# Optimization experiments

Hardware: AMD Instinct MI355X
Metric: run time of the kernel (lower is better)

The kernel has to match this reference:

```python
import jax, jax.numpy as jnp
import numpy as np

NT, NE = 2, 2            # node types, edge types
N, FIN, HID = 50000, 128, 128
H, D, L, E = 4, 32, 2, 400000
EDGE_SRC = (0, 1)        # edge type e: src node type
EDGE_DST = (1, 0)        # edge type e: dst node type


def _segment_softmax(scores, seg, n):
    # scores: [E, H], softmax over edges sharing the same dst node
    m = jax.ops.segment_max(scores, seg, num_segments=n)
    e = jnp.exp(scores - m[seg])
    s = jax.ops.segment_sum(e, seg, num_segments=n)
    return e / (s[seg] + 1e-16)


def setup_inputs() -> dict:
    key = jax.random.key(0)
    ks = iter(jax.random.split(key, 40))
    rn = lambda shape, sc=1.0: jax.random.normal(next(ks), shape, dtype=jnp.float32) * sc
    s_in, s_h, s_d = 1.0 / np.sqrt(FIN), 1.0 / np.sqrt(HID), 1.0 / np.sqrt(D)
    inp = {}
    inp["x"] = rn((NT, N, FIN))
    inp["ei"] = jax.random.randint(next(ks), (NE, 2, E), 0, N, dtype=jnp.int32)
    inp["ew"] = rn((NE, E))
    inp["lin_w"] = rn((NT, FIN, HID), s_in)
    inp["lin_b"] = jnp.zeros((NT, HID), jnp.float32)
    for nm in ("k", "q", "v", "a"):
        inp[nm + "_w"] = rn((L, NT, HID, HID), s_h)
        inp[nm + "_b"] = jnp.zeros((L, NT, HID), jnp.float32)
    inp["skip"] = jnp.ones((L, NT), jnp.float32)
    inp["rel_att"] = rn((L, NE, H, D, D), s_d)
    inp["rel_msg"] = rn((L, NE, H, D, D), s_d)
    inp["rel_p"] = jnp.ones((L, NE, H), jnp.float32)
    return inp


def reference(x, ei, ew, lin_w, lin_b, k_w, k_b, q_w, q_b, v_w, v_b,
              a_w, a_b, skip, rel_att, rel_msg, rel_p):
    inv_sqrt_d = jnp.float32(1.0 / np.sqrt(D))
    # per-node-type input projection + ReLU
    h = jax.nn.relu(jnp.einsum('tnf,tfh->tnh', x, lin_w) + lin_b[:, None, :])
    # sigmoid edge-weight scaling of source rows (last-write on duplicates, as torch *=)
    w = jax.nn.sigmoid(ew)  # [NE, E]
    for e in range(NE):
        s = EDGE_SRC[e]
        src = ei[e, 0]
        h = h.at[s, src].set(h[s, src] * w[e][:, None])
    for l in range(L):
        k = (jnp.einsum('tnh,tho->tno', h, k_w[l]) + k_b[l][:, None, :]).reshape(NT, N, H, D)
        q = (jnp.einsum('tnh,tho->tno', h, q_w[l]) + q_b[l][:, None, :]).reshape(NT, N, H, D)
        v = (jnp.einsum('tnh,tho->tno', h, v_w[l]) + v_b[l][:, None, :]).reshape(NT, N, H, D)
        agg = jnp.zeros((NT, N, H, D), h.dtype)
        for e in range(NE):
            s, t = EDGE_SRC[e], EDGE_DST[e]
            src, dst = ei[e, 0], ei[e, 1]
            k_rel = jnp.einsum('nhd,hde->nhe', k[s], rel_att[l, e])  # [N, H, D]
            v_rel = jnp.einsum('nhd,hde->nhe', v[s], rel_msg[l, e])
            alpha = jnp.einsum('ehd,ehd->eh', q[t][dst], k_rel[src]) * rel_p[l, e] * inv_sqrt_d
            alpha = _segment_softmax(alpha, dst, N)                  # [E, H]
            msg = v_rel[src] * alpha[:, :, None]                     # [E, H, D]
            agg = agg.at[t].add(jax.ops.segment_sum(msg, dst, num_segments=N))
        out = jnp.einsum('tnh,tho->tno', jax.nn.gelu(agg.reshape(NT, N, HID), approximate=False), a_w[l]) + a_b[l][:, None, :]
        beta = jax.nn.sigmoid(skip[l])[:, None, None]
        h = beta * out + (1.0 - beta) * h
    return h
```

## Files before the change

### kernel.cpp

```cpp
#include <hip/hip_runtime.h>
#include <hip/hip_bf16.h>
#include <math.h>

typedef __hip_bfloat16 bf16;
typedef _Float16 f16;
typedef __attribute__((ext_vector_type(2))) _Float16 f16x2;
typedef __attribute__((ext_vector_type(8))) short bf16x8;
typedef __attribute__((ext_vector_type(4))) float f32x4;
typedef __attribute__((ext_vector_type(4))) unsigned uivec4;

#define NT 2
#define NE 2
#define NN 50000
#define HID 128
#define NH 4
#define DD 32
#define NL 2
#define NEDGE 400000
#define MBLK64 782
#define AGGB 3125
#define WPITCH 136
#define CB 196
#define CAP 4096
#define CHUNK 2048
#define NCH 196

__device__ __forceinline__ float b2f(bf16 v) { return __bfloat162float(v); }
__device__ __forceinline__ float toF(float v) { return v; }
__device__ __forceinline__ float toF(bf16 v) { return b2f(v); }
__device__ __forceinline__ float sigm(float x) { return 1.0f / (1.0f + __expf(-x)); }
__device__ __forceinline__ unsigned short f2bits(float f) {
    bf16 h = __float2bfloat16(f);
    unsigned short b; __builtin_memcpy(&b, &h, 2); return b;
}
__device__ __forceinline__ float bits2f(unsigned short b) {
    unsigned u = ((unsigned)b) << 16; float f; __builtin_memcpy(&f, &u, 4); return f;
}
__device__ __forceinline__ unsigned short f2hbits(float f) {
    f16 h = (f16)f;
    unsigned short b; __builtin_memcpy(&b, &h, 2); return b;
}

__device__ __forceinline__ float dot8_f16(const unsigned* kr, const f16x2 q[4], float init) {
    float p = init;
#pragma unroll
    for (int i = 0; i < 4; i++) {
        f16x2 kh; __builtin_memcpy(&kh, &kr[i], 4);
#if __has_builtin(__builtin_amdgcn_fdot2)
        p = __builtin_amdgcn_fdot2(q[i], kh, p, false);
#else
        p += (float)q[i].x * (float)kh.x + (float)q[i].y * (float)kh.y;
#endif
    }
    return p;
}

__global__ void detect_kernel(const void* __restrict__ x, int* __restrict__ flag) {
    int lane = threadIdx.x;
    const unsigned short* u = (const unsigned short*)x;
    int cnt = 0;
    for (int i = 0; i < 4; i++) {
        unsigned short w = u[lane * 4 + i];
        int e = (w >> 7) & 0xFF;
        if (e >= 110 && e <= 135) cnt++;
    }
    for (int off = 32; off > 0; off >>= 1) cnt += __shfl_xor(cnt, off, 64);
    if (lane == 0) *flag = (cnt > 200) ? 0 : 1;
}

__global__ void bucket1_kernel(const int* __restrict__ ei, int* __restrict__ gcd,
                               int* __restrict__ gcs, unsigned* __restrict__ bufd,
                               unsigned* __restrict__ bufs) {
    int blk = blockIdx.x;
    int e = blk / NCH, ch = blk % NCH;
    int tid = threadIdx.x;
    __shared__ int hd[CB], hs[CB], bd[CB], bs[CB];
    for (int i = tid; i < CB; i += 256) { hd[i] = 0; hs[i] = 0; }
    __syncthreads();
    const int* srcp = ei + (e * 2 + 0) * NEDGE;
    const int* dstp = ei + (e * 2 + 1) * NEDGE;
    int j0 = ch * CHUNK;
    int src[8], dst[8], rd[8], rs[8];
#pragma unroll
    for (int i = 0; i < 8; i++) {
        int j = j0 + i * 256 + tid;
        if (j < NEDGE) {
            src[i] = srcp[j]; dst[i] = dstp[j];
            rd[i] = atomicAdd(&hd[dst[i] >> 8], 1);
            rs[i] = atomicAdd(&hs[src[i] >> 8], 1);
        } else src[i] = -1;
    }
    __syncthreads();
    for (int i = tid; i < CB; i += 256) {
        bd[i] = hd[i] ? atomicAdd(&gcd[e * CB + i], hd[i]) : 0;
        bs[i] = hs[i] ? atomicAdd(&gcs[e * CB + i], hs[i]) : 0;
    }
    __syncthreads();
#pragma unroll
    for (int i = 0; i < 8; i++) {
        int j = j0 + i * 256 + tid;
        if (j < NEDGE) {
            int bn = dst[i] >> 8;
            int pd = bd[bn] + rd[i]; if (pd >= CAP) pd = CAP - 1;
            bufd[((size_t)e * CB + bn) * CAP + pd] =
                ((unsigned)(dst[i] & 255) << 24) | (unsigned)src[i];
            bn = src[i] >> 8;
            int ps = bs[bn] + rs[i]; if (ps >= CAP) ps = CAP - 1;
            bufs[((size_t)e * CB + bn) * CAP + ps] =
                ((unsigned)(src[i] & 255) << 19) | (unsigned)j;
        }
    }
}

__global__ void cscan_kernel(const int* __restrict__ gcd, int* __restrict__ coff,
                             int* __restrict__ offs) {
    int e = blockIdx.x;
    int tid = threadIdx.x;
    __shared__ int sb[256];
    int v = (tid < CB) ? gcd[e * CB + tid] : 0;
    sb[tid] = v; __syncthreads();
    for (int off = 1; off < 256; off <<= 1) {
        int a = (tid >= off) ? sb[tid - off] : 0;
        __syncthreads();
        sb[tid] += a;
        __syncthreads();
    }
    if (tid < CB) coff[e * (CB + 1) + tid] = sb[tid] - v;
    if (tid == CB - 1) coff[e * (CB + 1) + CB] = sb[tid];
    if (tid == 0) offs[e * (NN + 1) + NN] = NEDGE;
}

__global__ void fine_dst_kernel(const unsigned* __restrict__ bufd, const int* __restrict__ gcd,
                                const int* __restrict__ coff, int* __restrict__ offs,
                                int* __restrict__ srcb) {
    int blk = blockIdx.x;
    int e = blk / CB, bn = blk % CB;
    int tid = threadIdx.x;
    int cnt = gcd[e * CB + bn]; if (cnt > CAP) cnt = CAP;
    int base = coff[e * (CB + 1) + bn];
    const unsigned* b = bufd + ((size_t)e * CB + bn) * CAP;
    __shared__ int dc[256], ss[256];
    dc[tid] = 0; __syncthreads();
    for (int i = tid; i < cnt; i += 256) atomicAdd(&dc[b[i] >> 24], 1);
    __syncthreads();
    int v = dc[tid];
    ss[tid] = v; __syncthreads();
    for (int off = 1; off < 256; off <<= 1) {
        int a = (tid >= off) ? ss[tid - off] : 0;
        __syncthreads();
        ss[tid] += a;
        __syncthreads();
    }
    int excl = ss[tid] - v;
    int d = bn * 256 + tid;
    if (d < NN) offs[e * (NN + 1) + d] = base + excl;
    dc[tid] = excl;
    __syncthreads();
    for (int i = tid; i < cnt; i += 256) {
        unsigned w = b[i];
        int r = atomicAdd(&dc[w >> 24], 1);
        srcb[(size_t)e * NEDGE + base + r] = (int)(w & 0xFFFFFF);
    }
}

__global__ void fine_src_kernel(const unsigned* __restrict__ bufs, const int* __restrict__ gcs,
                                const void* __restrict__ ew, float* __restrict__ ewsc,
                                const int* __restrict__ flag) {
    int blk = blockIdx.x;
    int e = blk / CB, bn = blk % CB;
    int tid = threadIdx.x;
    int cnt = gcs[e * CB + bn]; if (cnt > CAP) cnt = CAP;
    const unsigned* b = bufs + ((size_t)e * CB + bn) * CAP;
    __shared__ int mx[256];
    mx[tid] = -1; __syncthreads();
    for (int i = tid; i < cnt; i += 256) {
        unsigned w = b[i];
        atomicMax(&mx[w >> 19], (int)(w & 0x7FFFF));
    }
    __syncthreads();
    int n = bn * 256 + tid;
    if (n < NN) {
        int mj = mx[tid];
        float v = 1.0f;
        if (mj >= 0)
            v = sigm(*flag ? ((const float*)ew)[(size_t)e * NEDGE + mj]
                           : b2f(((const bf16*)ew)[(size_t)e * NEDGE + mj]));
        ewsc[e * NN + n] = v;
    }
}

template <typename T>
__device__ __forceinline__ void prep_w_body(const T* lin_w, const T* k_w, const T* q_w,
                                            const T* v_w, const T* a_w, const T* rel_att,
                                            const T* rel_msg, unsigned short* wT) {
    int bid = blockIdx.x, tid = threadIdx.x;
    int mat = bid >> 6;
    int elem = (bid & 63) * 256 + tid;
    int n = elem >> 7, k = elem & 127;
    float v;
    if (mat < 2) {
        v = toF(lin_w[(size_t)mat * 16384 + k * 128 + n]);
    } else if (mat < 14) {
        int m2 = mat - 2, lt = m2 / 3, op = m2 % 3;
        if (op == 1) {
            v = toF(q_w[(size_t)lt * 16384 + k * 128 + n]);
        } else {
            const T* w = (op == 0 ? k_w : v_w) + (size_t)lt * 16384 + k * 128;
            const T* rl = (op == 0 ? rel_att : rel_msg) + (size_t)lt * 4096;
            int hh = n >> 5, jj = n & 31;
            float s = 0.f;
#pragma unroll 8
            for (int d = 0; d < 32; d++)
                s += toF(w[hh * 32 + d]) * toF(rl[(hh * 32 + d) * 32 + jj]);
            v = s;
        }
    } else {
        v = toF(a_w[(size_t)(mat - 14) * 16384 + k * 128 + n]);
    }
    wT[(size_t)mat * 16384 + n * 128 + k] = f2bits(v);
}
__global__ void prep_w_kernel(const void* lin_w, const void* k_w, const void* q_w,
                              const void* v_w, const void* a_w, const void* rel_att,
                              const void* rel_msg, unsigned short* wT, const int* flag) {
    if (*flag) prep_w_body<float>((const float*)lin_w, (const float*)k_w, (const float*)q_w,
                                  (const float*)v_w, (const float*)a_w, (const float*)rel_att,
                                  (const float*)rel_msg, wT);
    else       prep_w_body<bf16>((const bf16*)lin_w, (const bf16*)k_w, (const bf16*)q_w,
                                 (const bf16*)v_w, (const bf16*)a_w, (const bf16*)rel_att,
                                 (const bf16*)rel_msg, wT);
}

template <typename T>
__device__ __forceinline__ void prep_misc_body(const T* lin_b, const T* k_b, const T* q_b,
                                               const T* v_b, const T* a_b, const T* rel_att,
                                               const T* rel_msg, const T* rel_p, const T* skip,
                                               float* biasall, float* relpf, float* skipf) {
    int mat = blockIdx.x, n = threadIdx.x;
    float v;
    if (mat < 2) {
        v = toF(lin_b[mat * 128 + n]);
    } else if (mat < 14) {
        int m2 = mat - 2, lt = m2 / 3, op = m2 % 3;
        if (op == 1) {
            v = toF(q_b[lt * 128 + n]);
        } else {
            const T* b = (op == 0 ? k_b : v_b) + lt * 128;
            const T* rl = (op == 0 ? rel_att : rel_msg) + (size_t)lt * 4096;
            int hh = n >> 5, jj = n & 31;
            float s = 0.f;
#pragma unroll 8
            for (int d = 0; d < 32; d++)
                s += toF(b[hh * 32 + d]) * toF(rl[(hh * 32 + d) * 32 + jj]);
            v = s;
        }
    } else {
        v = toF(a_b[(mat - 14) * 128 + n]);
    }
    biasall[mat * 128 + n] = v;
    if (mat == 0 && n < 16) relpf[n] = toF(rel_p[n]);
    if (mat == 1 && n < 4) skipf[n] = toF(skip[n]);
}
__global__ void prep_misc_kernel(const void* lin_b, const void* k_b, const void* q_b,
                                 const void* v_b, const void* a_b, const void* rel_att,
                                 const void* rel_msg, const void* rel_p, const void* skip,
                                 float* biasall, float* relpf, float* skipf, const int* flag) {
    if (*flag) prep_misc_body<float>((const float*)lin_b, (const float*)k_b, (const float*)q_b,
                                     (const float*)v_b, (const float*)a_b, (const float*)rel_att,
                                     (const float*)rel_msg, (const float*)rel_p, (const float*)skip,
                                     biasall, relpf, skipf);
    else       prep_misc_body<bf16>((const bf16*)lin_b, (const bf16*)k_b, (const bf16*)q_b,
                                    (const bf16*)v_b, (const bf16*)a_b, (const bf16*)rel_att,
                                    (const bf16*)rel_msg, (const bf16*)rel_p, (const bf16*)skip,
                                    biasall, relpf, skipf);
}

__device__ __forceinline__ void stage_w(unsigned short* __restrict__ Wl,
                                        const unsigned short* __restrict__ wmat, int tid) {
#pragma unroll
    for (int i = 0; i < 8; i++) {
        int c = i * 256 + tid;
        int n = c >> 4, ko = (c & 15) * 8;
        *(bf16x8*)&Wl[n * WPITCH + ko] = *(const bf16x8*)&wmat[n * 128 + ko];
    }
}

__device__ __forceinline__ void mfma_pass(const unsigned short* __restrict__ Wl,
                                          const bf16x8 af[4], const float* __restrict__ bias,
                                          f32x4 acc[8], int m16, int quad) {
#pragma unroll
    for (int ni = 0; ni < 8; ni++) {
        float b = bias[ni * 16 + m16];
        f32x4 iv = {b, b, b, b};
        acc[ni] = iv;
    }
#pragma unroll
    for (int ks = 0; ks < 4; ks++) {
        bf16x8 a = af[ks];
#pragma unroll
        for (int ni = 0; ni < 8; ni++) {
            bf16x8 bb = *(const bf16x8*)&Wl[(ni * 16 + m16) * WPITCH + ks * 32 + quad * 8];
            acc[ni] = __builtin_amdgcn_mfma_f32_16x16x32_bf16(a, bb, acc[ni], 0, 0, 0);
        }
    }
}

template <bool FP32>
__device__ __forceinline__ void lin_body(const void* __restrict__ x,
                                         const unsigned short* __restrict__ wT,
                                         const float* __restrict__ biasall,
                                         const float* __restrict__ ewsc,
                                         float* __restrict__ h) {
    __shared__ unsigned short Wl[128 * WPITCH];
    int bid = blockIdx.x, tid = threadIdx.x;
    int t = bid / MBLK64, nb = (bid % MBLK64) * 64;
    int wave = tid >> 6, lane = tid & 63;
    int m16 = lane & 15, quad = lane >> 4;
    stage_w(Wl, wT + (size_t)t * 16384, tid);
    int arow = nb + wave * 16 + m16;
    int arc = arow < NN ? arow : NN - 1;
    size_t abase = ((size_t)t * NN + arc) * 128;
    bf16x8 af[4];
#pragma unroll
    for (int ks = 0; ks < 4; ks++) {
        if (FP32) {
            const float4* s = (const float4*)((const float*)x + abase + ks * 32 + quad * 8);
            float4 f0 = s[0], f1 = s[1];
            unsigned short* pu = (unsigned short*)&af[ks];
            pu[0] = f2bits(f0.x); pu[1] = f2bits(f0.y); pu[2] = f2bits(f0.z); pu[3] = f2bits(f0.w);
            pu[4] = f2bits(f1.x); pu[5] = f2bits(f1.y); pu[6] = f2bits(f1.z); pu[7] = f2bits(f1.w);
        } else {
            af[ks] = *(const bf16x8*)((const unsigned short*)x + abase + ks * 32 + quad * 8);
        }
    }
    __syncthreads();
    f32x4 acc[8];
    mfma_pass(Wl, af, biasall + t * 128, acc, m16, quad);
#pragma unroll
    for (int r = 0; r < 4; r++) {
        int node = nb + wave * 16 + quad * 4 + r;
        if (node < NN) {
            float es = ewsc[t * NN + node];
            size_t ro = ((size_t)t * NN + node) * 128;
#pragma unroll
            for (int ni = 0; ni < 8; ni++)
                h[ro + ni * 16 + m16] = fmaxf(acc[ni][r], 0.f) * es;
        }
    }
}
__global__ void __launch_bounds__(256, 4) lin_gemm(const void* x, const unsigned short* wT,
                                                   const float* biasall, const float* ewsc,
                                                   float* h, const int* flag) {
    if (*flag) lin_body<true>(x, wT, biasall, ewsc, h);
    else       lin_body<false>(x, wT, biasall, ewsc, h);
}

__global__ void __launch_bounds__(256, 4) kqv_gemm(const float* __restrict__ h,
                                                   const unsigned short* __restrict__ wTall,
                                                   const float* __restrict__ biasall, int l,
                                                   unsigned short* __restrict__ kv,
                                                   unsigned short* __restrict__ qq) {
    __shared__ unsigned short Wl[128 * WPITCH];
    int bid = blockIdx.x, tid = threadIdx.x;
    int t = bid / MBLK64, nb = (bid % MBLK64) * 64;
    int lt = l * 2 + t;
    int wave = tid >> 6, lane = tid & 63;
    int m16 = lane & 15, quad = lane >> 4;
    int arow = nb + wave * 16 + m16;
    int arc = arow < NN ? arow : NN - 1;
    size_t abase = ((size_t)t * NN + arc) * 128;
    bf16x8 af[4];
#pragma unroll
    for (int ks = 0; ks < 4; ks++) {
        const float4* s = (const float4*)(h + abase + ks * 32 + quad * 8);
        float4 f0 = s[0], f1 = s[1];
        unsigned short* pu = (unsigned short*)&af[ks];
        pu[0] = f2bits(f0.x); pu[1] = f2bits(f0.y); pu[2] = f2bits(f0.z); pu[3] = f2bits(f0.w);
        pu[4] = f2bits(f1.x); pu[5] = f2bits(f1.y); pu[6] = f2bits(f1.z); pu[7] = f2bits(f1.w);
    }
    f32x4 acc[8];
#pragma unroll
    for (int pass = 0; pass < 3; pass++) {
        int mat = 2 + lt * 3 + pass;
        __syncthreads();
        stage_w(Wl, wTall + (size_t)mat * 16384, tid);
        __syncthreads();
        mfma_pass(Wl, af, biasall + mat * 128, acc, m16, quad);
#pragma unroll
        for (int r = 0; r < 4; r++) {
            int node = nb + wave * 16 + quad * 4 + r;
            if (node < NN) {
#pragma unroll
                for (int ni = 0; ni < 8; ni++) {
                    unsigned short hb = f2hbits(acc[ni][r]);
                    int c = ni * 16 + m16;
                    if (pass == 1) {
                        qq[((size_t)t * NN + node) * 128 + c] = hb;
                    } else {
                        size_t ro = ((size_t)t * NN + node) * 256 + (pass == 0 ? 0 : 128);
                        kv[ro + c] = hb;
                    }
                }
            }
        }
    }
}

__global__ void __launch_bounds__(256) agg_kernel(const unsigned short* __restrict__ qq,
                                                  const unsigned short* __restrict__ kv,
                                                  const int* __restrict__ srcb,
                                                  const int* __restrict__ offs,
                                                  const float* __restrict__ relpf, int l,
                                                  unsigned short* __restrict__ aggb) {
    int bid = blockIdx.x;
    int e = bid / AGGB;
    int wave = threadIdx.x >> 6, lane = threadIdx.x & 63;
    int stream = lane >> 4, l4 = lane & 15;
    int dst = (bid % AGGB) * 16 + wave * 4 + stream;
    int t = 1 - e;
    int le = l * 2 + e;
    int c0 = l4 * 8, head = l4 >> 2;
    const int* offs_e = offs + e * (NN + 1);
    const int* srcb_e = srcb + (size_t)e * NEDGE;
    int beg = offs_e[dst], end = offs_e[dst + 1];
    size_t rowo = ((size_t)t * NN + dst) * 128 + c0;
    float scale = relpf[le * 4 + head] * 0.17677669529663687f * 1.44269504088896f;
    uivec4 qraw = __builtin_nontemporal_load((const uivec4*)&qq[rowo]);
    f16x2 q[4];
#pragma unroll
    for (int i = 0; i < 4; i++) { unsigned w = qraw[i]; __builtin_memcpy(&q[i], &w, 4); }
    const unsigned short* kvb = kv + (size_t)e * NN * 256;
    float lsum = 0.f;
    float acc[8] = {0.f, 0.f, 0.f, 0.f, 0.f, 0.f, 0.f, 0.f};
    int jmax = end - 1;
    for (int j0 = beg; j0 < end; j0 += 4) {
        int src[4];
#pragma unroll
        for (int i = 0; i < 4; i++) {
            int j = j0 + i;
            src[i] = __builtin_nontemporal_load(&srcb_e[j <= jmax ? j : jmax]);
        }
        uivec4 kr[4], vr[4];
#pragma unroll
        for (int i = 0; i < 4; i++) {
            size_t so = (size_t)src[i] * 256 + c0;
            kr[i] = *(const uivec4*)&kvb[so];
            vr[i] = *(const uivec4*)&kvb[so + 128];
        }
#pragma unroll
        for (int i = 0; i < 4; i++) {
            float p = dot8_f16((const unsigned*)&kr[i], q, 0.f);
            p += __shfl_xor(p, 1, 64);
            p += __shfl_xor(p, 2, 64);
            float es = (j0 + i <= jmax) ? exp2f(p * scale) : 0.f;
            lsum += es;
            const unsigned* vu = (const unsigned*)&vr[i];
#pragma unroll
            for (int k = 0; k < 4; k++) {
                f16x2 vh; __builtin_memcpy(&vh, &vu[k], 4);
                acc[k * 2]     += es * (float)vh.x;
                acc[k * 2 + 1] += es * (float)vh.y;
            }
        }
    }
    float inv = 1.0f / (lsum + 1e-16f);
    unsigned short o[8];
#pragma unroll
    for (int i = 0; i < 8; i++) o[i] = f2bits(acc[i] * inv);
    *(bf16x8*)&aggb[rowo] = *(bf16x8*)o;
}

__global__ void __launch_bounds__(256, 4) outproj_gemm(const unsigned short* __restrict__ aggb,
                                                       const unsigned short* __restrict__ wTall,
                                                       const float* __restrict__ biasall,
                                                       const float* __restrict__ skipf, int l,
                                                       float* __restrict__ h, int last,
                                                       void* __restrict__ outp,
                                                       const int* __restrict__ flag) {
    __shared__ unsigned short Wl[128 * WPITCH];
    int bid = blockIdx.x, tid = threadIdx.x;
    int t = bid / MBLK64, nb = (bid % MBLK64) * 64;
    int lt = l * 2 + t;
    int wave = tid >> 6, lane = tid & 63;
    int m16 = lane & 15, quad = lane >> 4;
    int mat = 14 + lt;
    stage_w(Wl, wTall + (size_t)mat * 16384, tid);
    int arow = nb + wave * 16 + m16;
    int arc = arow < NN ? arow : NN - 1;
    size_t abase = ((size_t)t * NN + arc) * 128;
    bf16x8 af[4];
#pragma unroll
    for (int ks = 0; ks < 4; ks++) {
        bf16x8 raw = *(const bf16x8*)&aggb[abase + ks * 32 + quad * 8];
        const unsigned short* ru = (const unsigned short*)&raw;
        unsigned short* pu = (unsigned short*)&af[ks];
#pragma unroll
        for (int jj = 0; jj < 8; jj++) {
            float g = bits2f(ru[jj]);
            pu[jj] = f2bits(0.5f * g * (1.0f + erff(g * 0.70710678118654752f)));
        }
    }
    __syncthreads();
    f32x4 acc[8];
    mfma_pass(Wl, af, biasall + mat * 128, acc, m16, quad);
    float beta = sigm(skipf[lt]);
    int fl = *flag;
#pragma unroll
    for (int r = 0; r < 4; r++) {
        int node = nb + wave * 16 + quad * 4 + r;
        if (node < NN) {
            size_t ro = ((size_t)t * NN + node) * 128;
#pragma unroll
            for (int ni = 0; ni < 8; ni++) {
                size_t io = ro + ni * 16 + m16;
                float nv = beta * acc[ni][r] + (1.0f - beta) * h[io];
                h[io] = nv;
                if (last) {
                    if (fl) ((float*)outp)[io] = nv;
                    else    ((bf16*)outp)[io] = __float2bfloat16(nv);
                }
            }
        }
    }
}

extern "C" void kernel_launch(void* const* d_in, const int* in_sizes, int n_in,
                              void* d_out, int out_size, void* d_ws, size_t ws_size,
                              hipStream_t stream) {
    const void* x      = d_in[0];
    const int*  ei     = (const int*)d_in[1];
    const void* ew     = d_in[2];
    const void* lin_w  = d_in[3];
    const void* lin_b  = d_in[4];
    const void* k_w    = d_in[5];
    const void* k_b    = d_in[6];
    const void* q_w    = d_in[7];
    const void* q_b    = d_in[8];
    const void* v_w    = d_in[9];
    const void* v_b    = d_in[10];
    const void* a_w    = d_in[11];
    const void* a_b    = d_in[12];
    const void* skip   = d_in[13];
    const void* rel_att = d_in[14];
    const void* rel_msg = d_in[15];
    const void* rel_p  = d_in[16];

    char* p = (char*)d_ws;
    auto alloc = [&](size_t bytes) -> char* {
        char* r = p;
        p += (bytes + 255) & ~(size_t)255;
        return r;
    };
    int* flag     = (int*)alloc(sizeof(int));
    int* gcd      = (int*)alloc(sizeof(int) * NE * CB);
    int* gcs      = (int*)alloc(sizeof(int) * NE * CB);
    int* coff     = (int*)alloc(sizeof(int) * NE * (CB + 1));
    int* offs     = (int*)alloc(sizeof(int) * NE * (NN + 1));
    int* srcb     = (int*)alloc(sizeof(int) * NE * NEDGE);
    unsigned* bufd = (unsigned*)alloc(sizeof(unsigned) * NE * CB * CAP);
    unsigned* bufs = (unsigned*)alloc(sizeof(unsigned) * NE * CB * CAP);
    unsigned short* wTall = (unsigned short*)alloc(sizeof(short) * 18 * 16384);
    float* biasall = (float*)alloc(sizeof(float) * 18 * 128);
    float* relpf   = (float*)alloc(sizeof(float) * 16);
    float* skipf   = (float*)alloc(sizeof(float) * 4);
    float* ewsc    = (float*)alloc(sizeof(float) * NT * NN);
    float* h       = (float*)alloc(sizeof(float) * NT * NN * HID);
    unsigned short* qq = (unsigned short*)alloc(sizeof(short) * NT * NN * HID);
    unsigned short* kv = (unsigned short*)alloc(sizeof(short) * NT * NN * HID * 2);
    unsigned short* aggb = qq;

    hipMemsetAsync(gcd, 0, sizeof(int) * NE * CB, stream);
    hipMemsetAsync(gcs, 0, sizeof(int) * NE * CB, stream);

    detect_kernel<<<1, 64, 0, stream>>>(x, flag);
    bucket1_kernel<<<NE * NCH, 256, 0, stream>>>(ei, gcd, gcs, bufd, bufs);
    cscan_kernel<<<NE, 256, 0, stream>>>(gcd, coff, offs);
    fine_dst_kernel<<<NE * CB, 256, 0, stream>>>(bufd, gcd, coff, offs, srcb);
    fine_src_kernel<<<NE * CB, 256, 0, stream>>>(bufs, gcs, ew, ewsc, flag);
    prep_w_kernel<<<18 * 64, 256, 0, stream>>>(lin_w, k_w, q_w, v_w, a_w, rel_att, rel_msg,
                                               wTall, flag);
    prep_misc_kernel<<<18, 128, 0, stream>>>(lin_b, k_b, q_b, v_b, a_b, rel_att, rel_msg,
                                             rel_p, skip, biasall, relpf, skipf, flag);

    lin_gemm<<<NT * MBLK64, 256, 0, stream>>>(x, wTall, biasall, ewsc, h, flag);

    for (int l = 0; l < NL; l++) {
        kqv_gemm<<<NT * MBLK64, 256, 0, stream>>>(h, wTall, biasall, l, kv, qq);
        agg_kernel<<<NE * AGGB, 256, 0, stream>>>(qq, kv, srcb, offs, relpf, l, aggb);
        outproj_gemm<<<NT * MBLK64, 256, 0, stream>>>(aggb, wTall, biasall, skipf, l, h,
                                                      (l == NL - 1) ? 1 : 0, d_out, flag);
    }
}
```

Before: 446.7 us.

## Split aggregation into score and PV kernels with head-major K/Q/V layout

The KQV projection now writes K, Q and V into separate head-major arrays, one contiguous [N,32] table per node type and head, instead of interleaved K|V rows. The fused attention-aggregation kernel becomes two kernels. The first computes exp-scores per edge and head and stores them to a float buffer that reuses the bucketing scratch space. The second gathers V rows per head and does the weighted sum with normalization. The goal is to shrink each random gather to one head's 64B slice and keep per-head tables cache-resident, at the cost of an extra launch and a full write and read of the per-edge score buffer.

```diff
diff --git a/kernel.cpp b/kernel.cpp
--- a/kernel.cpp
+++ b/kernel.cpp
@@ -18,7 +18,7 @@
 #define NL 2
 #define NEDGE 400000
 #define MBLK64 782
-#define AGGB 3125
+#define PCHB 782
 #define WPITCH 136
 #define CB 196
 #define CAP 4096
@@ -357,8 +357,9 @@
 __global__ void __launch_bounds__(256, 4) kqv_gemm(const float* __restrict__ h,
                                                    const unsigned short* __restrict__ wTall,
                                                    const float* __restrict__ biasall, int l,
-                                                   unsigned short* __restrict__ kv,
-                                                   unsigned short* __restrict__ qq) {
+                                                   unsigned short* __restrict__ khead,
+                                                   unsigned short* __restrict__ qhead,
+                                                   unsigned short* __restrict__ vhead) {
     __shared__ unsigned short Wl[128 * WPITCH];
     int bid = blockIdx.x, tid = threadIdx.x;
     int t = bid / MBLK64, nb = (bid % MBLK64) * 64;
@@ -385,6 +386,7 @@
         stage_w(Wl, wTall + (size_t)mat * 16384, tid);
         __syncthreads();
         mfma_pass(Wl, af, biasall + mat * 128, acc, m16, quad);
+        unsigned short* dst0 = (pass == 0) ? khead : (pass == 1 ? qhead : vhead);
 #pragma unroll
         for (int r = 0; r < 4; r++) {
             int node = nb + wave * 16 + quad * 4 + r;
@@ -392,66 +394,100 @@
 #pragma unroll
                 for (int ni = 0; ni < 8; ni++) {
                     unsigned short hb = f2hbits(acc[ni][r]);
-                    int c = ni * 16 + m16;
-                    if (pass == 1) {
-                        qq[((size_t)t * NN + node) * 128 + c] = hb;
-                    } else {
-                        size_t ro = ((size_t)t * NN + node) * 256 + (pass == 0 ? 0 : 128);
-                        kv[ro + c] = hb;
-                    }
+                    int cch = ni * 16 + m16;
+                    int hh = cch >> 5, co = cch & 31;
+                    dst0[((size_t)(t * 4 + hh)) * NN * 32 + (size_t)node * 32 + co] = hb;
                 }
             }
         }
     }
 }
 
-__global__ void __launch_bounds__(256) agg_kernel(const unsigned short* __restrict__ qq,
-                                                  const unsigned short* __restrict__ kv,
-                                                  const int* __restrict__ srcb,
-                                                  const int* __restrict__ offs,
-                                                  const float* __restrict__ relpf, int l,
-                                                  unsigned short* __restrict__ aggb) {
+__global__ void __launch_bounds__(256) score_kernel(const unsigned short* __restrict__ qhead,
+                                                    const unsigned short* __restrict__ khead,
+                                                    const int* __restrict__ srcb,
+                                                    const int* __restrict__ offs,
+                                                    const float* __restrict__ relpf, int l,
+                                                    float* __restrict__ esb) {
     int bid = blockIdx.x;
-    int e = bid / AGGB;
-    int wave = threadIdx.x >> 6, lane = threadIdx.x & 63;
-    int stream = lane >> 4, l4 = lane & 15;
-    int dst = (bid % AGGB) * 16 + wave * 4 + stream;
-    int t = 1 - e;
-    int le = l * 2 + e;
-    int c0 = l4 * 8, head = l4 >> 2;
+    int combo = bid & 7, chunk = bid >> 3;
+    int e = combo >> 2, hh = combo & 3, t = 1 - e;
+    int group = threadIdx.x >> 2, c = threadIdx.x & 3;
+    int dst = chunk * 64 + group;
+    if (dst >= NN) return;
     const int* offs_e = offs + e * (NN + 1);
     const int* srcb_e = srcb + (size_t)e * NEDGE;
+    const unsigned short* kt = khead + ((size_t)(e * 4 + hh)) * NN * 32;
+    const unsigned short* qt = qhead + ((size_t)(t * 4 + hh)) * NN * 32;
+    float* esb_eh = esb + (size_t)combo * NEDGE;
+    float scale = relpf[(l * 2 + e) * 4 + hh] * 0.17677669529663687f * 1.44269504088896f;
     int beg = offs_e[dst], end = offs_e[dst + 1];
-    size_t rowo = ((size_t)t * NN + dst) * 128 + c0;
-    float scale = relpf[le * 4 + head] * 0.17677669529663687f * 1.44269504088896f;
-    uivec4 qraw = __builtin_nontemporal_load((const uivec4*)&qq[rowo]);
+    uivec4 qraw = __builtin_nontemporal_load((const uivec4*)&qt[(size_t)dst * 32 + c * 8]);
     f16x2 q[4];
 #pragma unroll
     for (int i = 0; i < 4; i++) { unsigned w = qraw[i]; __builtin_memcpy(&q[i], &w, 4); }
-    const unsigned short* kvb = kv + (size_t)e * NN * 256;
-    float lsum = 0.f;
-    float acc[8] = {0.f, 0.f, 0.f, 0.f, 0.f, 0.f, 0.f, 0.f};
-    int jmax = end - 1;
     for (int j0 = beg; j0 < end; j0 += 4) {
         int src[4];
 #pragma unroll
         for (int i = 0; i < 4; i++) {
             int j = j0 + i;
-            src[i] = __builtin_nontemporal_load(&srcb_e[j <= jmax ? j : jmax]);
-        }
-        uivec4 kr[4], vr[4];
-#pragma unroll
-        for (int i = 0; i < 4; i++) {
-            size_t so = (size_t)src[i] * 256 + c0;
-            kr[i] = *(const uivec4*)&kvb[so];
-            vr[i] = *(const uivec4*)&kvb[so + 128];
-        }
+            src[i] = __builtin_nontemporal_load(&srcb_e[j < end ? j : end - 1]);
+        }
+        uivec4 kr[4];
+#pragma unroll
+        for (int i = 0; i < 4; i++)
+            kr[i] = *(const uivec4*)&kt[(size_t)src[i] * 32 + c * 8];
+        float es0 = 0.f, es1 = 0.f, es2 = 0.f, es3 = 0.f;
 #pragma unroll
         for (int i = 0; i < 4; i++) {
             float p = dot8_f16((const unsigned*)&kr[i], q, 0.f);
             p += __shfl_xor(p, 1, 64);
             p += __shfl_xor(p, 2, 64);
-            float es = (j0 + i <= jmax) ? exp2f(p * scale) : 0.f;
+            float es = exp2f(p * scale);
+            if (i == 0) es0 = es; else if (i == 1) es1 = es;
+            else if (i == 2) es2 = es; else es3 = es;
+        }
+        float mye = (c == 0) ? es0 : (c == 1) ? es1 : (c == 2) ? es2 : es3;
+        int j = j0 + c;
+        if (j < end) __builtin_nontemporal_store(mye, &esb_eh[j]);
+    }
+}
+
+__global__ void __launch_bounds__(256) pv_kernel(const unsigned short* __restrict__ vhead,
+                                                 const int* __restrict__ srcb,
+                                                 const int* __restrict__ offs,
+                                                 const float* __restrict__ esb,
+                                                 unsigned short* __restrict__ aggb) {
+    int bid = blockIdx.x;
+    int combo = bid & 7, chunk = bid >> 3;
+    int e = combo >> 2, hh = combo & 3, t = 1 - e;
+    int group = threadIdx.x >> 2, c = threadIdx.x & 3;
+    int dst = chunk * 64 + group;
+    if (dst >= NN) return;
+    const int* offs_e = offs + e * (NN + 1);
+    const int* srcb_e = srcb + (size_t)e * NEDGE;
+    const unsigned short* vt = vhead + ((size_t)(e * 4 + hh)) * NN * 32;
+    const float* esb_eh = esb + (size_t)combo * NEDGE;
+    int beg = offs_e[dst], end = offs_e[dst + 1];
+    float lsum = 0.f;
+    float acc[8] = {0.f, 0.f, 0.f, 0.f, 0.f, 0.f, 0.f, 0.f};
+    for (int j0 = beg; j0 < end; j0 += 4) {
+        int src[4]; float esr[4];
+#pragma unroll
+        for (int i = 0; i < 4; i++) {
+            int j = j0 + i;
+            int jc = j < end ? j : end - 1;
+            src[i] = __builtin_nontemporal_load(&srcb_e[jc]);
+            float ev = __builtin_nontemporal_load(&esb_eh[jc]);
+            esr[i] = (j < end) ? ev : 0.f;
+        }
+        uivec4 vr[4];
+#pragma unroll
+        for (int i = 0; i < 4; i++)
+            vr[i] = *(const uivec4*)&vt[(size_t)src[i] * 32 + c * 8];
+#pragma unroll
+        for (int i = 0; i < 4; i++) {
+            float es = esr[i];
             lsum += es;
             const unsigned* vu = (const unsigned*)&vr[i];
 #pragma unroll
@@ -466,7 +502,7 @@
     unsigned short o[8];
 #pragma unroll
     for (int i = 0; i < 8; i++) o[i] = f2bits(acc[i] * inv);
-    *(bf16x8*)&aggb[rowo] = *(bf16x8*)o;
+    *(bf16x8*)&aggb[((size_t)t * NN + dst) * 128 + hh * 32 + c * 8] = *(bf16x8*)o;
 }
 
 __global__ void __launch_bounds__(256, 4) outproj_gemm(const unsigned short* __restrict__ aggb,
@@ -564,9 +600,11 @@
     float* skipf   = (float*)alloc(sizeof(float) * 4);
     float* ewsc    = (float*)alloc(sizeof(float) * NT * NN);
     float* h       = (float*)alloc(sizeof(float) * NT * NN * HID);
-    unsigned short* qq = (unsigned short*)alloc(sizeof(short) * NT * NN * HID);
-    unsigned short* kv = (unsigned short*)alloc(sizeof(short) * NT * NN * HID * 2);
-    unsigned short* aggb = qq;
+    unsigned short* khead = (unsigned short*)alloc(sizeof(short) * NT * NH * NN * 32);
+    unsigned short* qhead = (unsigned short*)alloc(sizeof(short) * NT * NH * NN * 32);
+    unsigned short* vhead = (unsigned short*)alloc(sizeof(short) * NT * NH * NN * 32);
+    float* esb = (float*)bufd;
+    unsigned short* aggb = qhead;
 
     hipMemsetAsync(gcd, 0, sizeof(int) * NE * CB, stream);
     hipMemsetAsync(gcs, 0, sizeof(int) * NE * CB, stream);
@@ -584,8 +622,9 @@
     lin_gemm<<<NT * MBLK64, 256, 0, stream>>>(x, wTall, biasall, ewsc, h, flag);
 
     for (int l = 0; l < NL; l++) {
-        kqv_gemm<<<NT * MBLK64, 256, 0, stream>>>(h, wTall, biasall, l, kv, qq);
-        agg_kernel<<<NE * AGGB, 256, 0, stream>>>(qq, kv, srcb, offs, relpf, l, aggb);
+        kqv_gemm<<<NT * MBLK64, 256, 0, stream>>>(h, wTall, biasall, l, khead, qhead, vhead);
+        score_kernel<<<PCHB * 8, 256, 0, stream>>>(qhead, khead, srcb, offs, relpf, l, esb);
+        pv_kernel<<<PCHB * 8, 256, 0, stream>>>(vhead, srcb, offs, esb, aggb);
         outproj_gemm<<<NT * MBLK64, 256, 0, stream>>>(aggb, wTall, biasall, skipf, l, h,
                                                       (l == NL - 1) ? 1 : 0, d_out, flag);
     }
```

Result: slower. 549.2 us (+22.9%).

## Fuse input projection and output projection with following layer's K/Q/V GEMM

Applied to the files above, without the earlier changes.

Merges the input projection GEMM with layer-0 K/Q/V projection, and layer-0 output projection with layer-1 K/Q/V projection. The freshly computed h tile is kept in shared memory as bf16 and fed straight into the K/Q/V MFMA passes. This avoids re-reading the fp32 h array from global memory and saves two kernel launches. In exchange it adds an extra shared tile, lowers the launch-bounds occupancy hint from 4 to 3, and relies on each block reading its aggb rows (aliased with qq) before overwriting them.

```diff
diff --git a/kernel.cpp b/kernel.cpp
--- a/kernel.cpp
+++ b/kernel.cpp
@@ -304,79 +304,17 @@
     }
 }
 
-template <bool FP32>
-__device__ __forceinline__ void lin_body(const void* __restrict__ x,
-                                         const unsigned short* __restrict__ wT,
-                                         const float* __restrict__ biasall,
-                                         const float* __restrict__ ewsc,
-                                         float* __restrict__ h) {
-    __shared__ unsigned short Wl[128 * WPITCH];
-    int bid = blockIdx.x, tid = threadIdx.x;
-    int t = bid / MBLK64, nb = (bid % MBLK64) * 64;
-    int wave = tid >> 6, lane = tid & 63;
-    int m16 = lane & 15, quad = lane >> 4;
-    stage_w(Wl, wT + (size_t)t * 16384, tid);
-    int arow = nb + wave * 16 + m16;
-    int arc = arow < NN ? arow : NN - 1;
-    size_t abase = ((size_t)t * NN + arc) * 128;
-    bf16x8 af[4];
-#pragma unroll
-    for (int ks = 0; ks < 4; ks++) {
-        if (FP32) {
-            const float4* s = (const float4*)((const float*)x + abase + ks * 32 + quad * 8);
-            float4 f0 = s[0], f1 = s[1];
-            unsigned short* pu = (unsigned short*)&af[ks];
-            pu[0] = f2bits(f0.x); pu[1] = f2bits(f0.y); pu[2] = f2bits(f0.z); pu[3] = f2bits(f0.w);
-            pu[4] = f2bits(f1.x); pu[5] = f2bits(f1.y); pu[6] = f2bits(f1.z); pu[7] = f2bits(f1.w);
-        } else {
-            af[ks] = *(const bf16x8*)((const unsigned short*)x + abase + ks * 32 + quad * 8);
-        }
-    }
-    __syncthreads();
-    f32x4 acc[8];
-    mfma_pass(Wl, af, biasall + t * 128, acc, m16, quad);
-#pragma unroll
-    for (int r = 0; r < 4; r++) {
-        int node = nb + wave * 16 + quad * 4 + r;
-        if (node < NN) {
-            float es = ewsc[t * NN + node];
-            size_t ro = ((size_t)t * NN + node) * 128;
-#pragma unroll
-            for (int ni = 0; ni < 8; ni++)
-                h[ro + ni * 16 + m16] = fmaxf(acc[ni][r], 0.f) * es;
-        }
-    }
-}
-__global__ void __launch_bounds__(256, 4) lin_gemm(const void* x, const unsigned short* wT,
-                                                   const float* biasall, const float* ewsc,
-                                                   float* h, const int* flag) {
-    if (*flag) lin_body<true>(x, wT, biasall, ewsc, h);
-    else       lin_body<false>(x, wT, biasall, ewsc, h);
-}
-
-__global__ void __launch_bounds__(256, 4) kqv_gemm(const float* __restrict__ h,
-                                                   const unsigned short* __restrict__ wTall,
-                                                   const float* __restrict__ biasall, int l,
-                                                   unsigned short* __restrict__ kv,
-                                                   unsigned short* __restrict__ qq) {
-    __shared__ unsigned short Wl[128 * WPITCH];
-    int bid = blockIdx.x, tid = threadIdx.x;
-    int t = bid / MBLK64, nb = (bid % MBLK64) * 64;
-    int lt = l * 2 + t;
-    int wave = tid >> 6, lane = tid & 63;
-    int m16 = lane & 15, quad = lane >> 4;
-    int arow = nb + wave * 16 + m16;
-    int arc = arow < NN ? arow : NN - 1;
-    size_t abase = ((size_t)t * NN + arc) * 128;
-    bf16x8 af[4];
-#pragma unroll
-    for (int ks = 0; ks < 4; ks++) {
-        const float4* s = (const float4*)(h + abase + ks * 32 + quad * 8);
-        float4 f0 = s[0], f1 = s[1];
-        unsigned short* pu = (unsigned short*)&af[ks];
-        pu[0] = f2bits(f0.x); pu[1] = f2bits(f0.y); pu[2] = f2bits(f0.z); pu[3] = f2bits(f0.w);
-        pu[4] = f2bits(f1.x); pu[5] = f2bits(f1.y); pu[6] = f2bits(f1.z); pu[7] = f2bits(f1.w);
-    }
+__device__ __forceinline__ void kqv_passes(const unsigned short* __restrict__ hT,
+                                           unsigned short* __restrict__ Wl,
+                                           const unsigned short* __restrict__ wTall,
+                                           const float* __restrict__ biasall, int lt,
+                                           unsigned short* __restrict__ kv,
+                                           unsigned short* __restrict__ qq,
+                                           int t, int nb, int wave, int m16, int quad, int tid) {
+    bf16x8 af2[4];
+#pragma unroll
+    for (int ks = 0; ks < 4; ks++)
+        af2[ks] = *(const bf16x8*)&hT[(wave * 16 + m16) * WPITCH + ks * 32 + quad * 8];
     f32x4 acc[8];
 #pragma unroll
     for (int pass = 0; pass < 3; pass++) {
@@ -384,7 +322,7 @@
         __syncthreads();
         stage_w(Wl, wTall + (size_t)mat * 16384, tid);
         __syncthreads();
-        mfma_pass(Wl, af, biasall + mat * 128, acc, m16, quad);
+        mfma_pass(Wl, af2, biasall + mat * 128, acc, m16, quad);
 #pragma unroll
         for (int r = 0; r < 4; r++) {
             int node = nb + wave * 16 + quad * 4 + r;
@@ -403,6 +341,65 @@
             }
         }
     }
+}
+
+template <bool FP32>
+__device__ __forceinline__ void lin_kqv_body(const void* __restrict__ x,
+                                             const unsigned short* __restrict__ wTall,
+                                             const float* __restrict__ biasall,
+                                             const float* __restrict__ ewsc,
+                                             float* __restrict__ h,
+                                             unsigned short* __restrict__ kv,
+                                             unsigned short* __restrict__ qq) {
+    __shared__ unsigned short Wl[128 * WPITCH];
+    __shared__ unsigned short hT[64 * WPITCH];
+    int bid = blockIdx.x, tid = threadIdx.x;
+    int t = bid / MBLK64, nb = (bid % MBLK64) * 64;
+    int wave = tid >> 6, lane = tid & 63;
+    int m16 = lane & 15, quad = lane >> 4;
+    stage_w(Wl, wTall + (size_t)t * 16384, tid);
+    int arow = nb + wave * 16 + m16;
+    int arc = arow < NN ? arow : NN - 1;
+    size_t abase = ((size_t)t * NN + arc) * 128;
+    bf16x8 af[4];
+#pragma unroll
+    for (int ks = 0; ks < 4; ks++) {
+        if (FP32) {
+            const float4* s = (const float4*)((const float*)x + abase + ks * 32 + quad * 8);
+            float4 f0 = s[0], f1 = s[1];
+            unsigned short* pu = (unsigned short*)&af[ks];
+            pu[0] = f2bits(f0.x); pu[1] = f2bits(f0.y); pu[2] = f2bits(f0.z); pu[3] = f2bits(f0.w);
+            pu[4] = f2bits(f1.x); pu[5] = f2bits(f1.y); pu[6] = f2bits(f1.z); pu[7] = f2bits(f1.w);
+        } else {
+            af[ks] = *(const bf16x8*)((const unsigned short*)x + abase + ks * 32 + quad * 8);
+        }
+    }
+    __syncthreads();
+    f32x4 acc[8];
+    mfma_pass(Wl, af, biasall + t * 128, acc, m16, quad);
+#pragma unroll
+    for (int r = 0; r < 4; r++) {
+        int rloc = wave * 16 + quad * 4 + r;
+        int node = nb + rloc;
+        float es = ewsc[t * NN + (node < NN ? node : NN - 1)];
+#pragma unroll
+        for (int ni = 0; ni < 8; ni++) {
+            float v = fmaxf(acc[ni][r], 0.f) * es;
+            unsigned short vb = (node < NN) ? f2bits(v) : (unsigned short)0;
+            if (node < NN) h[((size_t)t * NN + node) * 128 + ni * 16 + m16] = v;
+            hT[rloc * WPITCH + ni * 16 + m16] = vb;
+        }
+    }
+    __syncthreads();
+    kqv_passes(hT, Wl, wTall, biasall, t, kv, qq, t, nb, wave, m16, quad, tid);
+}
+__global__ void __launch_bounds__(256, 3) lin_kqv_gemm(const void* x,
+                                                       const unsigned short* wTall,
+                                                       const float* biasall, const float* ewsc,
+                                                       float* h, unsigned short* kv,
+                                                       unsigned short* qq, const int* flag) {
+    if (*flag) lin_kqv_body<true>(x, wTall, biasall, ewsc, h, kv, qq);
+    else       lin_kqv_body<false>(x, wTall, biasall, ewsc, h, kv, qq);
 }
 
 __global__ void __launch_bounds__(256) agg_kernel(const unsigned short* __restrict__ qq,
@@ -467,6 +464,61 @@
 #pragma unroll
     for (int i = 0; i < 8; i++) o[i] = f2bits(acc[i] * inv);
     *(bf16x8*)&aggb[rowo] = *(bf16x8*)o;
+}
+
+__global__ void __launch_bounds__(256, 3) outproj_kqv_gemm(const unsigned short* __restrict__ aggb,
+                                                           const unsigned short* __restrict__ wTall,
+                                                           const float* __restrict__ biasall,
+                                                           const float* __restrict__ skipf, int l,
+                                                           float* __restrict__ h,
+                                                           unsigned short* __restrict__ kv,
+                                                           unsigned short* __restrict__ qq) {
+    __shared__ unsigned short Wl[128 * WPITCH];
+    __shared__ unsigned short hT[64 * WPITCH];
+    int bid = blockIdx.x, tid = threadIdx.x;
+    int t = bid / MBLK64, nb = (bid % MBLK64) * 64;
+    int lt = l * 2 + t;
+    int wave = tid >> 6, lane = tid & 63;
+    int m16 = lane & 15, quad = lane >> 4;
+    int mat = 14 + lt;
+    stage_w(Wl, wTall + (size_t)mat * 16384, tid);
+    int arow = nb + wave * 16 + m16;
+    int arc = arow < NN ? arow : NN - 1;
+    size_t abase = ((size_t)t * NN + arc) * 128;
+    bf16x8 af[4];
+#pragma unroll
+    for (int ks = 0; ks < 4; ks++) {
+        bf16x8 raw = *(const bf16x8*)&aggb[abase + ks * 32 + quad * 8];
+        const unsigned short* ru = (const unsigned short*)&raw;
+        unsigned short* pu = (unsigned short*)&af[ks];
+#pragma unroll
+        for (int jj = 0; jj < 8; jj++) {
+            float g = bits2f(ru[jj]);
+            pu[jj] = f2bits(0.5f * g * (1.0f + erff(g * 0.70710678118654752f)));
+        }
+    }
+    __syncthreads();
+    f32x4 acc[8];
+    mfma_pass(Wl, af, biasall + mat * 128, acc, m16, quad);
+    float beta = sigm(skipf[lt]);
+#pragma unroll
+    for (int r = 0; r < 4; r++) {
+        int rloc = wave * 16 + quad * 4 + r;
+        int node = nb + rloc;
+#pragma unroll
+        for (int ni = 0; ni < 8; ni++) {
+            unsigned short vb = 0;
+            if (node < NN) {
+                size_t io = ((size_t)t * NN + node) * 128 + ni * 16 + m16;
+                float nv = beta * acc[ni][r] + (1.0f - beta) * h[io];
+                h[io] = nv;
+                vb = f2bits(nv);
+            }
+            hT[rloc * WPITCH + ni * 16 + m16] = vb;
+        }
+    }
+    __syncthreads();
+    kqv_passes(hT, Wl, wTall, biasall, (l + 1) * 2 + t, kv, qq, t, nb, wave, m16, quad, tid);
 }
 
 __global__ void __launch_bounds__(256, 4) outproj_gemm(const unsigned short* __restrict__ aggb,
@@ -581,12 +633,10 @@
     prep_misc_kernel<<<18, 128, 0, stream>>>(lin_b, k_b, q_b, v_b, a_b, rel_att, rel_msg,
                                              rel_p, skip, biasall, relpf, skipf, flag);
 
-    lin_gemm<<<NT * MBLK64, 256, 0, stream>>>(x, wTall, biasall, ewsc, h, flag);
-
-    for (int l = 0; l < NL; l++) {
-        kqv_gemm<<<NT * MBLK64, 256, 0, stream>>>(h, wTall, biasall, l, kv, qq);
-        agg_kernel<<<NE * AGGB, 256, 0, stream>>>(qq, kv, srcb, offs, relpf, l, aggb);
-        outproj_gemm<<<NT * MBLK64, 256, 0, stream>>>(aggb, wTall, biasall, skipf, l, h,
-                                                      (l == NL - 1) ? 1 : 0, d_out, flag);
-    }
-}
+    lin_kqv_gemm<<<NT * MBLK64, 256, 0, stream>>>(x, wTall, biasall, ewsc, h, kv, qq, flag);
+    agg_kernel<<<NE * AGGB, 256, 0, stream>>>(qq, kv, srcb, offs, relpf, 0, aggb);
+    outproj_kqv_gemm<<<NT * MBLK64, 256, 0, stream>>>(aggb, wTall, biasall, skipf, 0, h, kv, qq);
+    agg_kernel<<<NE * AGGB, 256, 0, stream>>>(qq, kv, srcb, offs, relpf, 1, aggb);
+    outproj_gemm<<<NT * MBLK64, 256, 0, stream>>>(aggb, wTall, biasall, skipf, 1, h, 1,
+                                                  d_out, flag);
+}
```

Measured after the change: 452.9 us. About the same (+1.4%).
